# Optimization experiments

Hardware: AMD Instinct MI355X
Metric: run time of the kernel (lower is better)

The kernel has to match this reference:

```python
import jax, jax.numpy as jnp
import numpy as np

N_NODES = 100000
IN_CH = 128
HID = 128   # 2 * out_channels
OUT = 64
N_EDGES = 1600000


def gcn_conv(x, W, b, src, dst, n_nodes):
    """PyG GCNConv: add self-loops, symmetric normalization D^-1/2 (A+I) D^-1/2 X W + b."""
    h = x @ W  # [N, F_out]
    ones = jnp.ones(dst.shape[0], dtype=h.dtype)
    # degree of target nodes, +1 for self loop
    deg = jax.ops.segment_sum(ones, dst, num_segments=n_nodes) + 1.0
    dinv = jnp.where(deg > 0, jax.lax.rsqrt(deg), 0.0)  # [N]
    norm = dinv[src] * dinv[dst]  # [E]
    agg = jax.ops.segment_sum(h[src] * norm[:, None], dst, num_segments=n_nodes)
    # self-loop contribution: norm_ii = dinv_i^2 (avoids materializing extra edges)
    agg = agg + h * (dinv * dinv)[:, None]
    return agg + b


def setup_inputs() -> dict:
    key = jax.random.key(0)
    ks = jax.random.split(key, 8)
    x = jax.random.normal(ks[0], (N_NODES, IN_CH), dtype=jnp.float32)
    edge_index = jax.random.randint(ks[1], (2, N_EDGES), 0, N_NODES, dtype=jnp.int64)
    # Glorot-style params
    W1 = jax.random.normal(ks[2], (IN_CH, HID), dtype=jnp.float32) / np.sqrt(IN_CH)
    b1 = jnp.zeros((HID,), dtype=jnp.float32)
    W_mu = jax.random.normal(ks[3], (HID, OUT), dtype=jnp.float32) / np.sqrt(HID)
    b_mu = jnp.zeros((OUT,), dtype=jnp.float32)
    W_ls = jax.random.normal(ks[4], (HID, OUT), dtype=jnp.float32) / np.sqrt(HID)
    b_ls = jnp.zeros((OUT,), dtype=jnp.float32)
    return {"x": x, "edge_index": edge_index, "W1": W1, "b1": b1,
            "W_mu": W_mu, "b_mu": b_mu, "W_ls": W_ls, "b_ls": b_ls}


def reference(x, edge_index, W1, b1, W_mu, b_mu, W_ls, b_ls):
    src, dst = edge_index[0], edge_index[1]
    n = x.shape[0]
    h = jax.nn.relu(gcn_conv(x, W1, b1, src, dst, n))
    mu = gcn_conv(h, W_mu, b_mu, src, dst, n)
    logstd = gcn_conv(h, W_ls, b_ls, src, dst, n)
    return (mu, logstd)
```

## Files before the change

### kernel.cpp

```cpp
#include <hip/hip_runtime.h>
#include <hip/hip_bf16.h>
#include <stdint.h>

#define N_NODES 100000
#define IN_CH   128
#define HID     128
#define OUT_CH  64
#define N_EDGES 1600000

#define NB    196
#define NBLK  250
#define EPB   6400

typedef __attribute__((ext_vector_type(8))) short  bf16x8;
typedef __attribute__((ext_vector_type(4))) float  f32x4;


__device__ __forceinline__ unsigned short f2bf(float f) {
    unsigned int u = __float_as_uint(f);
    u = (u + 0x7fffu + ((u >> 16) & 1u)) >> 16;
    return (unsigned short)u;
}
__device__ __forceinline__ float bfl(unsigned int u) { return __uint_as_float(u << 16); }
__device__ __forceinline__ float bfh(unsigned int u) { return __uint_as_float(u & 0xffff0000u); }


__global__ __launch_bounds__(256) void k_phaseA(const int* __restrict__ dst,
                                                int* __restrict__ Cm) {
    __shared__ int hist[NB];
    int blk = blockIdx.x, t = threadIdx.x;
    if (t < NB) hist[t] = 0;
    __syncthreads();
    int base = blk * EPB;
#pragma unroll 5
    for (int k = 0; k < EPB / 256; k++) {
        int d = dst[base + k * 256 + t];
        atomicAdd(&hist[d >> 9], 1);
    }
    __syncthreads();
    if (t < NB) Cm[blk * NB + t] = hist[t];
}

__global__ __launch_bounds__(256) void k_scanBkt(int* __restrict__ Cm,
                                                 int* __restrict__ bktSum) {
    __shared__ int sdata[256];
    int b = blockIdx.x, t = threadIdx.x;
    int v = (t < NBLK) ? Cm[t * NB + b] : 0;
    sdata[t] = v;
    __syncthreads();
    int val = v;
    for (int off = 1; off < 256; off <<= 1) {
        int tmp = (t >= off) ? sdata[t - off] : 0;
        __syncthreads();
        val += tmp;
        sdata[t] = val;
        __syncthreads();
    }
    if (t < NBLK) Cm[t * NB + b] = val - v;
    if (t == 255) bktSum[b] = val;
}

__global__ __launch_bounds__(256) void k_scanBase(const int* __restrict__ bktSum,
                                                  int* __restrict__ bktBase) {
    __shared__ int sdata[256];
    int t = threadIdx.x;
    int v = (t < NB) ? bktSum[t] : 0;
    sdata[t] = v;
    __syncthreads();
    int val = v;
    for (int off = 1; off < 256; off <<= 1) {
        int tmp = (t >= off) ? sdata[t - off] : 0;
        __syncthreads();
        val += tmp;
        sdata[t] = val;
        __syncthreads();
    }
    if (t < NB) bktBase[t] = val - v;
    if (t == 0) bktBase[NB] = N_EDGES;
}

__global__ __launch_bounds__(256) void k_phaseB(const int* __restrict__ src,
                                                const int* __restrict__ dst,
                                                const int* __restrict__ Cm,
                                                const int* __restrict__ bktBase,
                                                unsigned int* __restrict__ bucketed) {
    __shared__ int offs[NB];
    int blk = blockIdx.x, t = threadIdx.x;
    if (t < NB) offs[t] = Cm[blk * NB + t] + bktBase[t];
    __syncthreads();
    int base = blk * EPB;
#pragma unroll 5
    for (int k = 0; k < EPB / 256; k++) {
        int e = base + k * 256 + t;
        int d = dst[e];
        int sv = src[e];
        int pos = atomicAdd(&offs[d >> 9], 1);
        bucketed[pos] = ((unsigned int)sv << 9) | (unsigned int)(d & 511);
    }
}

__global__ __launch_bounds__(512) void k_phaseC(const unsigned int* __restrict__ bucketed,
                                                const int* __restrict__ bktBase,
                                                int* __restrict__ rowptr,
                                                float* __restrict__ dinvg,
                                                int* __restrict__ csr_src) {
    __shared__ int cnt[512];
    __shared__ int cur[512];
    __shared__ int sdata[512];
    int b = blockIdx.x, t = threadIdx.x;
    int base = bktBase[b], endR = bktBase[b + 1];
    int nodeBase = b << 9;
    int nNodes = N_NODES - nodeBase;
    if (nNodes > 512) nNodes = 512;

    cnt[t] = 0;
    __syncthreads();
    for (int e = base + t; e < endR; e += 512)
        atomicAdd(&cnt[bucketed[e] & 511], 1);
    __syncthreads();

    int s = cnt[t];
    sdata[t] = s;
    __syncthreads();
    int val = s;
    for (int off = 1; off < 512; off <<= 1) {
        int tmp = (t >= off) ? sdata[t - off] : 0;
        __syncthreads();
        val += tmp;
        sdata[t] = val;
        __syncthreads();
    }
    cur[t] = val - s;
    if (t < nNodes) {
        rowptr[nodeBase + t] = base + val - s;
        dinvg[nodeBase + t] = rsqrtf((float)s + 1.0f);
    }
    if (b == NB - 1 && t == 0) rowptr[N_NODES] = N_EDGES;
    __syncthreads();

    for (int e = base + t; e < endR; e += 512) {
        unsigned int u = bucketed[e];
        int pos = base + atomicAdd(&cur[u & 511], 1);
        csr_src[pos] = (int)(u >> 9);
    }
}


__global__ __launch_bounds__(256) void k_prepW(const float* __restrict__ W1,
                                               const float* __restrict__ Wmu,
                                               const float* __restrict__ Wls,
                                               unsigned short* __restrict__ Wt1,
                                               unsigned short* __restrict__ WtC) {
    int idx = blockIdx.x * 256 + threadIdx.x;
    int n = idx >> 7, k = idx & 127;
    Wt1[idx] = f2bf(W1[k * 128 + n]);
    WtC[idx] = f2bf((n < 64) ? Wmu[k * 64 + n] : Wls[k * 64 + (n - 64)]);
}


#define LDA 136

__global__ __launch_bounds__(256) void k_gemm1(const float* __restrict__ X,
                                               const unsigned short* __restrict__ Wt,
                                               unsigned short* __restrict__ Y) {
    __shared__ unsigned short sA[128 * LDA];
    int t = threadIdx.x;
    int R0 = blockIdx.x * 128;
    int row = t >> 1, colb = (t & 1) * 64;
    bool valid = (R0 + row) < N_NODES;
    const float* Xr = X + (size_t)(R0 + row) * 128 + colb;
    unsigned short* dp = sA + row * LDA + colb;
#pragma unroll
    for (int j = 0; j < 16; j++) {
        float4 v = valid ? *(const float4*)(Xr + j * 4) : make_float4(0.f, 0.f, 0.f, 0.f);
        ushort4 o;
        o.x = f2bf(v.x); o.y = f2bf(v.y); o.z = f2bf(v.z); o.w = f2bf(v.w);
        *(ushort4*)(dp + j * 4) = o;
    }
    __syncthreads();

    int wv = t >> 6, l = t & 63;
    int quad = l >> 4, lm = l & 15;

    bf16x8 a[2][4];
#pragma unroll
    for (int mt = 0; mt < 2; mt++)
#pragma unroll
        for (int ks = 0; ks < 4; ks++)
            a[mt][ks] = *(const bf16x8*)(sA + (wv * 32 + mt * 16 + lm) * LDA +
                                         ks * 32 + quad * 8);

    f32x4 acc[2][8] = {};
#pragma unroll
    for (int nt = 0; nt < 8; nt++) {
        bf16x8 b[4];
        const unsigned short* Wp = Wt + (nt * 16 + lm) * 128 + quad * 8;
#pragma unroll
        for (int ks = 0; ks < 4; ks++)
            b[ks] = *(const bf16x8*)(Wp + ks * 32);
#pragma unroll
        for (int mt = 0; mt < 2; mt++) {
            f32x4 c = acc[mt][nt];
#pragma unroll
            for (int ks = 0; ks < 4; ks++)
                c = __builtin_amdgcn_mfma_f32_16x16x32_bf16(a[mt][ks], b[ks], c, 0, 0, 0);
            acc[mt][nt] = c;
        }
    }

    int rbase = R0 + wv * 32 + quad * 4;
#pragma unroll
    for (int mt = 0; mt < 2; mt++)
#pragma unroll
        for (int nt = 0; nt < 8; nt++)
#pragma unroll
            for (int reg = 0; reg < 4; reg++) {
                int r = rbase + mt * 16 + reg;
                if (r < N_NODES)
                    Y[(size_t)r * 128 + nt * 16 + lm] = f2bf(acc[mt][nt][reg]);
            }
}


__global__ __launch_bounds__(256) void k_agg1(const unsigned short* __restrict__ h0,
                                              const int* __restrict__ rowptr,
                                              const int* __restrict__ csr_src,
                                              const float* __restrict__ dinv,
                                              const float* __restrict__ b1,
                                              unsigned short* __restrict__ hb) {
    int lane = threadIdx.x & 63;
    int i = __builtin_amdgcn_readfirstlane(blockIdx.x * 4 + (threadIdx.x >> 6));
    int c2 = lane * 2;
    float di = dinv[i];
    unsigned int sv = *(const unsigned int*)(h0 + (size_t)i * 128 + c2);
    float ax = bfl(sv) * di * di, ay = bfh(sv) * di * di;
    int beg = rowptr[i], end = rowptr[i + 1];
    for (int p = beg; p < end; p += 16) {
        int s[16]; float n[16]; unsigned int r[16];
#pragma unroll
        for (int j = 0; j < 16; j++) {
            int q = p + j;
            s[j] = csr_src[q < end ? q : end - 1];
        }
#pragma unroll
        for (int j = 0; j < 16; j++) n[j] = dinv[s[j]];
#pragma unroll
        for (int j = 0; j < 16; j++)
            r[j] = *(const unsigned int*)(h0 + (size_t)s[j] * 128 + c2);
#pragma unroll
        for (int j = 0; j < 16; j++) n[j] = (p + j < end) ? n[j] * di : 0.f;
#pragma unroll
        for (int j = 0; j < 16; j++) {
            ax = fmaf(bfl(r[j]), n[j], ax);
            ay = fmaf(bfh(r[j]), n[j], ay);
        }
    }
    ax += b1[c2];
    ay += b1[c2 + 1];
    ax = ax > 0.f ? ax : 0.f;
    ay = ay > 0.f ? ay : 0.f;
    unsigned int pk = ((unsigned int)f2bf(ay) << 16) | (unsigned int)f2bf(ax);
    *(unsigned int*)(hb + (size_t)i * 128 + c2) = pk;
}


#define LDG 136

__global__ __launch_bounds__(256) void k_agg2g(const unsigned short* __restrict__ hb,
                                               const int* __restrict__ rowptr,
                                               const int* __restrict__ csr_src,
                                               const float* __restrict__ dinv,
                                               const unsigned short* __restrict__ WtC,
                                               const float* __restrict__ bmu,
                                               const float* __restrict__ bls,
                                               float* __restrict__ out) {
    __shared__ unsigned short g[16 * LDG];
    int t = threadIdx.x;
    int wv = t >> 6, lane = t & 63;
    int nodeBase = blockIdx.x * 16;
    int c2 = lane * 2;

#pragma unroll 1
    for (int j4 = 0; j4 < 4; j4++) {
        int i = __builtin_amdgcn_readfirstlane(nodeBase + wv * 4 + j4);
        float di = dinv[i];
        unsigned int sv = *(const unsigned int*)(hb + (size_t)i * 128 + c2);
        float ax = bfl(sv) * di * di, ay = bfh(sv) * di * di;
        int beg = rowptr[i], end = rowptr[i + 1];
        for (int p = beg; p < end; p += 16) {
            int s[16]; float n[16]; unsigned int r[16];
#pragma unroll
            for (int j = 0; j < 16; j++) {
                int q = p + j;
                s[j] = csr_src[q < end ? q : end - 1];
            }
#pragma unroll
            for (int j = 0; j < 16; j++) n[j] = dinv[s[j]];
#pragma unroll
            for (int j = 0; j < 16; j++)
                r[j] = *(const unsigned int*)(hb + (size_t)s[j] * 128 + c2);
#pragma unroll
            for (int j = 0; j < 16; j++) n[j] = (p + j < end) ? n[j] * di : 0.f;
#pragma unroll
            for (int j = 0; j < 16; j++) {
                ax = fmaf(bfl(r[j]), n[j], ax);
                ay = fmaf(bfh(r[j]), n[j], ay);
            }
        }
        unsigned int pk = ((unsigned int)f2bf(ay) << 16) | (unsigned int)f2bf(ax);
        *(unsigned int*)(g + (wv * 4 + j4) * LDG + c2) = pk;
    }
    __syncthreads();

    int quad = lane >> 4, lm = lane & 15;
    bf16x8 a[4];
#pragma unroll
    for (int ks = 0; ks < 4; ks++)
        a[ks] = *(const bf16x8*)(g + lm * LDG + ks * 32 + quad * 8);

#pragma unroll
    for (int nt2 = 0; nt2 < 2; nt2++) {
        int nt = wv * 2 + nt2;
        f32x4 acc = {};
        const unsigned short* Wp = WtC + (nt * 16 + lm) * 128 + quad * 8;
#pragma unroll
        for (int ks = 0; ks < 4; ks++) {
            bf16x8 b = *(const bf16x8*)(Wp + ks * 32);
            acc = __builtin_amdgcn_mfma_f32_16x16x32_bf16(a[ks], b, acc, 0, 0, 0);
        }
        int col = nt * 16 + lm;
#pragma unroll
        for (int reg = 0; reg < 4; reg++) {
            int row = nodeBase + quad * 4 + reg;
            float v = acc[reg];
            if (col < 64)
                out[(size_t)row * 64 + col] = v + bmu[col];
            else
                out[(size_t)N_NODES * 64 + (size_t)row * 64 + (col - 64)] = v + bls[col - 64];
        }
    }
}


extern "C" void kernel_launch(void* const* d_in, const int* in_sizes, int n_in,
                              void* d_out, int out_size, void* d_ws, size_t ws_size,
                              hipStream_t stream) {
    const float* x    = (const float*)d_in[0];
    const int*   ei   = (const int*)d_in[1];
    const float* W1   = (const float*)d_in[2];
    const float* b1   = (const float*)d_in[3];
    const float* Wmu  = (const float*)d_in[4];
    const float* bmu  = (const float*)d_in[5];
    const float* Wls  = (const float*)d_in[6];
    const float* bls  = (const float*)d_in[7];
    const int* src = ei;
    const int* dst = ei + N_EDGES;

    char* p = (char*)d_ws;
    unsigned short* bufA = (unsigned short*)p; p += (size_t)N_NODES * 128 * 2;
    unsigned short* bufH = (unsigned short*)p; p += (size_t)N_NODES * 128 * 2;
    unsigned short* Wt1  = (unsigned short*)p; p += 128 * 128 * 2;
    unsigned short* WtC  = (unsigned short*)p; p += 128 * 128 * 2;
    int*   Cm      = (int*)p;   p += (size_t)NBLK * NB * 4;
    int*   bktSum  = (int*)p;   p += 256 * 4;
    int*   bktBase = (int*)p;   p += 256 * 4;
    int*   rowptr  = (int*)p;   p += 400016;
    float* dinv    = (float*)p; p += 400000;
    unsigned int* bucketed = (unsigned int*)p; p += (size_t)N_EDGES * 4;
    int*   csr_src = (int*)p;   p += (size_t)N_EDGES * 4;

    k_phaseA<<<NBLK, 256, 0, stream>>>(dst, Cm);
    k_scanBkt<<<NB, 256, 0, stream>>>(Cm, bktSum);
    k_scanBase<<<1, 256, 0, stream>>>(bktSum, bktBase);
    k_phaseB<<<NBLK, 256, 0, stream>>>(src, dst, Cm, bktBase, bucketed);
    k_phaseC<<<NB, 512, 0, stream>>>(bucketed, bktBase, rowptr, dinv, csr_src);

    k_prepW<<<64, 256, 0, stream>>>(W1, Wmu, Wls, Wt1, WtC);

    int gblk = (N_NODES + 127) / 128;

    k_gemm1<<<gblk, 256, 0, stream>>>(x, Wt1, bufA);
    k_agg1<<<N_NODES / 4, 256, 0, stream>>>(bufA, rowptr, csr_src, dinv, b1, bufH);

    k_agg2g<<<N_NODES / 16, 256, 0, stream>>>(bufH, rowptr, csr_src, dinv,
                                              WtC, bmu, bls, (float*)d_out);
}
```

Measured before the change: 360.8 us.

## Slice feature matrices into 16-column planes for cache-local sparse aggregation

Result: slower. 756.1 us (+109.6%).

```diff
diff --git a/kernel.cpp b/kernel.cpp
--- a/kernel.cpp
+++ b/kernel.cpp
@@ -217,128 +217,159 @@
             for (int reg = 0; reg < 4; reg++) {
                 int r = rbase + mt * 16 + reg;
                 if (r < N_NODES)
-                    Y[(size_t)r * 128 + nt * 16 + lm] = f2bf(acc[mt][nt][reg]);
+                    Y[((size_t)nt * N_NODES + r) * 16 + lm] = f2bf(acc[mt][nt][reg]);
             }
 }
 
 
-__global__ __launch_bounds__(256) void k_agg1(const unsigned short* __restrict__ h0,
+template<int LAYER>
+__global__ __launch_bounds__(256) void k_aggs(const unsigned short* __restrict__ Hin,
                                               const int* __restrict__ rowptr,
                                               const int* __restrict__ csr_src,
                                               const float* __restrict__ dinv,
-                                              const float* __restrict__ b1,
-                                              unsigned short* __restrict__ hb) {
-    int lane = threadIdx.x & 63;
-    int i = __builtin_amdgcn_readfirstlane(blockIdx.x * 4 + (threadIdx.x >> 6));
-    int c2 = lane * 2;
-    float di = dinv[i];
-    unsigned int sv = *(const unsigned int*)(h0 + (size_t)i * 128 + c2);
-    float ax = bfl(sv) * di * di, ay = bfh(sv) * di * di;
-    int beg = rowptr[i], end = rowptr[i + 1];
-    for (int p = beg; p < end; p += 16) {
-        int s[16]; float n[16]; unsigned int r[16];
-#pragma unroll
-        for (int j = 0; j < 16; j++) {
-            int q = p + j;
-            s[j] = csr_src[q < end ? q : end - 1];
+                                              const float* __restrict__ bias,
+                                              unsigned short* __restrict__ Hout) {
+    int t = threadIdx.x;
+    int wv = t >> 6, l = t & 63;
+    int slice = blockIdx.x & 7;
+    int blkn = blockIdx.x >> 3;
+    int quad = l >> 2, ql = l & 3;
+    int i = blkn * 64 + wv * 16 + quad;
+    bool vnode = i < N_NODES;
+    int il = vnode ? i : 0;
+    const unsigned short* Hs = Hin + (size_t)slice * (N_NODES * 16);
+
+    float di = dinv[il];
+    int beg = vnode ? rowptr[il] : 0;
+    int end = vnode ? rowptr[il + 1] : 0;
+    int deg = end - beg;
+
+    int md = deg;
+    md = max(md, __shfl_xor(md, 4));
+    md = max(md, __shfl_xor(md, 8));
+    md = max(md, __shfl_xor(md, 16));
+    md = max(md, __shfl_xor(md, 32));
+    md = __builtin_amdgcn_readfirstlane(md);
+
+    uint2 sv = *(const uint2*)(Hs + (size_t)il * 16 + ql * 4);
+    float nn = di * di;
+    float a0 = bfl(sv.x) * nn, a1 = bfh(sv.x) * nn;
+    float a2 = bfl(sv.y) * nn, a3 = bfh(sv.y) * nn;
+
+    for (int p = 0; p < md; p += 8) {
+        int s[8]; float n[8]; uint2 r[8];
+#pragma unroll
+        for (int j = 0; j < 8; j++) {
+            int q = beg + p + j;
+            int qc = q < end ? q : end - 1;
+            qc = qc < 0 ? 0 : qc;
+            s[j] = __builtin_nontemporal_load(csr_src + qc);
         }
 #pragma unroll
-        for (int j = 0; j < 16; j++) n[j] = dinv[s[j]];
-#pragma unroll
-        for (int j = 0; j < 16; j++)
-            r[j] = *(const unsigned int*)(h0 + (size_t)s[j] * 128 + c2);
-#pragma unroll
-        for (int j = 0; j < 16; j++) n[j] = (p + j < end) ? n[j] * di : 0.f;
-#pragma unroll
-        for (int j = 0; j < 16; j++) {
-            ax = fmaf(bfl(r[j]), n[j], ax);
-            ay = fmaf(bfh(r[j]), n[j], ay);
+        for (int j = 0; j < 8; j++) n[j] = dinv[s[j]];
+#pragma unroll
+        for (int j = 0; j < 8; j++)
+            r[j] = *(const uint2*)(Hs + (size_t)s[j] * 16 + ql * 4);
+#pragma unroll
+        for (int j = 0; j < 8; j++) n[j] = (beg + p + j < end) ? n[j] * di : 0.f;
+#pragma unroll
+        for (int j = 0; j < 8; j++) {
+            a0 = fmaf(bfl(r[j].x), n[j], a0);
+            a1 = fmaf(bfh(r[j].x), n[j], a1);
+            a2 = fmaf(bfl(r[j].y), n[j], a2);
+            a3 = fmaf(bfh(r[j].y), n[j], a3);
         }
     }
-    ax += b1[c2];
-    ay += b1[c2 + 1];
-    ax = ax > 0.f ? ax : 0.f;
-    ay = ay > 0.f ? ay : 0.f;
-    unsigned int pk = ((unsigned int)f2bf(ay) << 16) | (unsigned int)f2bf(ax);
-    *(unsigned int*)(hb + (size_t)i * 128 + c2) = pk;
-}
-
-
-#define LDG 136
-
-__global__ __launch_bounds__(256) void k_agg2g(const unsigned short* __restrict__ hb,
-                                               const int* __restrict__ rowptr,
-                                               const int* __restrict__ csr_src,
-                                               const float* __restrict__ dinv,
-                                               const unsigned short* __restrict__ WtC,
+
+    if (!vnode) return;
+
+    if (LAYER == 1) {
+        const float4 bv = *(const float4*)(bias + slice * 16 + ql * 4);
+        a0 += bv.x; a1 += bv.y; a2 += bv.z; a3 += bv.w;
+        a0 = a0 > 0.f ? a0 : 0.f;
+        a1 = a1 > 0.f ? a1 : 0.f;
+        a2 = a2 > 0.f ? a2 : 0.f;
+        a3 = a3 > 0.f ? a3 : 0.f;
+        uint2 o;
+        o.x = ((unsigned int)f2bf(a1) << 16) | (unsigned int)f2bf(a0);
+        o.y = ((unsigned int)f2bf(a3) << 16) | (unsigned int)f2bf(a2);
+        *(uint2*)(Hout + ((size_t)slice * N_NODES + i) * 16 + ql * 4) = o;
+    } else {
+        uint2 o;
+        o.x = ((unsigned int)f2bf(a1) << 16) | (unsigned int)f2bf(a0);
+        o.y = ((unsigned int)f2bf(a3) << 16) | (unsigned int)f2bf(a2);
+        *(uint2*)(Hout + (size_t)i * 128 + slice * 16 + ql * 4) = o;
+    }
+}
+
+
+__global__ __launch_bounds__(256) void k_gemm2(const unsigned short* __restrict__ G,
+                                               const unsigned short* __restrict__ Wt,
                                                const float* __restrict__ bmu,
                                                const float* __restrict__ bls,
                                                float* __restrict__ out) {
-    __shared__ unsigned short g[16 * LDG];
+    __shared__ unsigned short sA[128 * LDA];
     int t = threadIdx.x;
-    int wv = t >> 6, lane = t & 63;
-    int nodeBase = blockIdx.x * 16;
-    int c2 = lane * 2;
-
-#pragma unroll 1
-    for (int j4 = 0; j4 < 4; j4++) {
-        int i = __builtin_amdgcn_readfirstlane(nodeBase + wv * 4 + j4);
-        float di = dinv[i];
-        unsigned int sv = *(const unsigned int*)(hb + (size_t)i * 128 + c2);
-        float ax = bfl(sv) * di * di, ay = bfh(sv) * di * di;
-        int beg = rowptr[i], end = rowptr[i + 1];
-        for (int p = beg; p < end; p += 16) {
-            int s[16]; float n[16]; unsigned int r[16];
-#pragma unroll
-            for (int j = 0; j < 16; j++) {
-                int q = p + j;
-                s[j] = csr_src[q < end ? q : end - 1];
-            }
-#pragma unroll
-            for (int j = 0; j < 16; j++) n[j] = dinv[s[j]];
-#pragma unroll
-            for (int j = 0; j < 16; j++)
-                r[j] = *(const unsigned int*)(hb + (size_t)s[j] * 128 + c2);
-#pragma unroll
-            for (int j = 0; j < 16; j++) n[j] = (p + j < end) ? n[j] * di : 0.f;
-#pragma unroll
-            for (int j = 0; j < 16; j++) {
-                ax = fmaf(bfl(r[j]), n[j], ax);
-                ay = fmaf(bfh(r[j]), n[j], ay);
+    int R0 = blockIdx.x * 128;
+    int row = t >> 1, colb = (t & 1) * 64;
+    bool valid = (R0 + row) < N_NODES;
+    const unsigned short* Gr = G + (size_t)(R0 + row) * 128 + colb;
+    unsigned short* dp = sA + row * LDA + colb;
+#pragma unroll
+    for (int j = 0; j < 8; j++) {
+        bf16x8 v = {0, 0, 0, 0, 0, 0, 0, 0};
+        if (valid) v = *(const bf16x8*)(Gr + j * 8);
+        *(bf16x8*)(dp + j * 8) = v;
+    }
+    __syncthreads();
+
+    int wv = t >> 6, l = t & 63;
+    int quad = l >> 4, lm = l & 15;
+
+    bf16x8 a[2][4];
+#pragma unroll
+    for (int mt = 0; mt < 2; mt++)
+#pragma unroll
+        for (int ks = 0; ks < 4; ks++)
+            a[mt][ks] = *(const bf16x8*)(sA + (wv * 32 + mt * 16 + lm) * LDA +
+                                         ks * 32 + quad * 8);
+
+    f32x4 acc[2][8] = {};
+#pragma unroll
+    for (int nt = 0; nt < 8; nt++) {
+        bf16x8 b[4];
+        const unsigned short* Wp = Wt + (nt * 16 + lm) * 128 + quad * 8;
+#pragma unroll
+        for (int ks = 0; ks < 4; ks++)
+            b[ks] = *(const bf16x8*)(Wp + ks * 32);
+#pragma unroll
+        for (int mt = 0; mt < 2; mt++) {
+            f32x4 c = acc[mt][nt];
+#pragma unroll
+            for (int ks = 0; ks < 4; ks++)
+                c = __builtin_amdgcn_mfma_f32_16x16x32_bf16(a[mt][ks], b[ks], c, 0, 0, 0);
+            acc[mt][nt] = c;
+        }
+    }
+
+    int rbase = R0 + wv * 32 + quad * 4;
+#pragma unroll
+    for (int mt = 0; mt < 2; mt++)
+#pragma unroll
+        for (int nt = 0; nt < 8; nt++) {
+            int col = nt * 16 + lm;
+#pragma unroll
+            for (int reg = 0; reg < 4; reg++) {
+                int r = rbase + mt * 16 + reg;
+                if (r < N_NODES) {
+                    float v = acc[mt][nt][reg];
+                    if (col < 64)
+                        out[(size_t)r * 64 + col] = v + bmu[col];
+                    else
+                        out[(size_t)N_NODES * 64 + (size_t)r * 64 + (col - 64)] = v + bls[col - 64];
+                }
             }
         }
-        unsigned int pk = ((unsigned int)f2bf(ay) << 16) | (unsigned int)f2bf(ax);
-        *(unsigned int*)(g + (wv * 4 + j4) * LDG + c2) = pk;
-    }
-    __syncthreads();
-
-    int quad = lane >> 4, lm = lane & 15;
-    bf16x8 a[4];
-#pragma unroll
-    for (int ks = 0; ks < 4; ks++)
-        a[ks] = *(const bf16x8*)(g + lm * LDG + ks * 32 + quad * 8);
-
-#pragma unroll
-    for (int nt2 = 0; nt2 < 2; nt2++) {
-        int nt = wv * 2 + nt2;
-        f32x4 acc = {};
-        const unsigned short* Wp = WtC + (nt * 16 + lm) * 128 + quad * 8;
-#pragma unroll
-        for (int ks = 0; ks < 4; ks++) {
-            bf16x8 b = *(const bf16x8*)(Wp + ks * 32);
-            acc = __builtin_amdgcn_mfma_f32_16x16x32_bf16(a[ks], b, acc, 0, 0, 0);
-        }
-        int col = nt * 16 + lm;
-#pragma unroll
-        for (int reg = 0; reg < 4; reg++) {
-            int row = nodeBase + quad * 4 + reg;
-            float v = acc[reg];
-            if (col < 64)
-                out[(size_t)row * 64 + col] = v + bmu[col];
-            else
-                out[(size_t)N_NODES * 64 + (size_t)row * 64 + (col - 64)] = v + bls[col - 64];
-        }
-    }
 }
 
 
@@ -378,10 +409,11 @@
     k_prepW<<<64, 256, 0, stream>>>(W1, Wmu, Wls, Wt1, WtC);
 
     int gblk = (N_NODES + 127) / 128;
+    int aggblk = ((N_NODES + 63) / 64) * 8;
 
     k_gemm1<<<gblk, 256, 0, stream>>>(x, Wt1, bufA);
-    k_agg1<<<N_NODES / 4, 256, 0, stream>>>(bufA, rowptr, csr_src, dinv, b1, bufH);
-
-    k_agg2g<<<N_NODES / 16, 256, 0, stream>>>(bufH, rowptr, csr_src, dinv,
-                                              WtC, bmu, bls, (float*)d_out);
-}
+    k_aggs<1><<<aggblk, 256, 0, stream>>>(bufA, rowptr, csr_src, dinv, b1, bufH);
+
+    k_aggs<2><<<aggblk, 256, 0, stream>>>(bufH, rowptr, csr_src, dinv, bmu, bufA);
+    k_gemm2<<<gblk, 256, 0, stream>>>(bufA, WtC, bmu, bls, (float*)d_out);
+}
```

## Fold source-side degree normalization into producers and drop per-edge dinv gathers

Applied to the files above, without the earlier changes.

New measurement: 348.2 us. 3.5% less time.

```diff
diff --git a/kernel.cpp b/kernel.cpp
--- a/kernel.cpp
+++ b/kernel.cpp
@@ -162,6 +162,7 @@
 
 __global__ __launch_bounds__(256) void k_gemm1(const float* __restrict__ X,
                                                const unsigned short* __restrict__ Wt,
+                                               const float* __restrict__ dinv,
                                                unsigned short* __restrict__ Y) {
     __shared__ unsigned short sA[128 * LDA];
     int t = threadIdx.x;
@@ -209,6 +210,14 @@
     }
 
     int rbase = R0 + wv * 32 + quad * 4;
+    float dv[2][4];
+#pragma unroll
+    for (int mt = 0; mt < 2; mt++)
+#pragma unroll
+        for (int reg = 0; reg < 4; reg++) {
+            int r = rbase + mt * 16 + reg;
+            dv[mt][reg] = (r < N_NODES) ? dinv[r] : 0.f;
+        }
 #pragma unroll
     for (int mt = 0; mt < 2; mt++)
 #pragma unroll
@@ -217,7 +226,7 @@
             for (int reg = 0; reg < 4; reg++) {
                 int r = rbase + mt * 16 + reg;
                 if (r < N_NODES)
-                    Y[(size_t)r * 128 + nt * 16 + lm] = f2bf(acc[mt][nt][reg]);
+                    Y[(size_t)r * 128 + nt * 16 + lm] = f2bf(acc[mt][nt][reg] * dv[mt][reg]);
             }
 }
 
@@ -233,32 +242,31 @@
     int c2 = lane * 2;
     float di = dinv[i];
     unsigned int sv = *(const unsigned int*)(h0 + (size_t)i * 128 + c2);
-    float ax = bfl(sv) * di * di, ay = bfh(sv) * di * di;
+    float ax = bfl(sv), ay = bfh(sv);
     int beg = rowptr[i], end = rowptr[i + 1];
-    for (int p = beg; p < end; p += 16) {
-        int s[16]; float n[16]; unsigned int r[16];
-#pragma unroll
-        for (int j = 0; j < 16; j++) {
+    for (int p = beg; p < end; p += 32) {
+        int s[32]; unsigned int r[32];
+#pragma unroll
+        for (int j = 0; j < 32; j++) {
             int q = p + j;
             s[j] = csr_src[q < end ? q : end - 1];
         }
 #pragma unroll
-        for (int j = 0; j < 16; j++) n[j] = dinv[s[j]];
-#pragma unroll
-        for (int j = 0; j < 16; j++)
+        for (int j = 0; j < 32; j++)
             r[j] = *(const unsigned int*)(h0 + (size_t)s[j] * 128 + c2);
 #pragma unroll
-        for (int j = 0; j < 16; j++) n[j] = (p + j < end) ? n[j] * di : 0.f;
-#pragma unroll
-        for (int j = 0; j < 16; j++) {
-            ax = fmaf(bfl(r[j]), n[j], ax);
-            ay = fmaf(bfh(r[j]), n[j], ay);
-        }
-    }
-    ax += b1[c2];
-    ay += b1[c2 + 1];
+        for (int j = 0; j < 32; j++) {
+            unsigned int v = (p + j < end) ? r[j] : 0u;
+            ax += bfl(v);
+            ay += bfh(v);
+        }
+    }
+    ax = ax * di + b1[c2];
+    ay = ay * di + b1[c2 + 1];
     ax = ax > 0.f ? ax : 0.f;
     ay = ay > 0.f ? ay : 0.f;
+    ax *= di;
+    ay *= di;
     unsigned int pk = ((unsigned int)f2bf(ay) << 16) | (unsigned int)f2bf(ax);
     *(unsigned int*)(hb + (size_t)i * 128 + c2) = pk;
 }
@@ -285,28 +293,27 @@
         int i = __builtin_amdgcn_readfirstlane(nodeBase + wv * 4 + j4);
         float di = dinv[i];
         unsigned int sv = *(const unsigned int*)(hb + (size_t)i * 128 + c2);
-        float ax = bfl(sv) * di * di, ay = bfh(sv) * di * di;
+        float ax = bfl(sv), ay = bfh(sv);
         int beg = rowptr[i], end = rowptr[i + 1];
-        for (int p = beg; p < end; p += 16) {
-            int s[16]; float n[16]; unsigned int r[16];
-#pragma unroll
-            for (int j = 0; j < 16; j++) {
+        for (int p = beg; p < end; p += 32) {
+            int s[32]; unsigned int r[32];
+#pragma unroll
+            for (int j = 0; j < 32; j++) {
                 int q = p + j;
                 s[j] = csr_src[q < end ? q : end - 1];
             }
 #pragma unroll
-            for (int j = 0; j < 16; j++) n[j] = dinv[s[j]];
-#pragma unroll
-            for (int j = 0; j < 16; j++)
+            for (int j = 0; j < 32; j++)
                 r[j] = *(const unsigned int*)(hb + (size_t)s[j] * 128 + c2);
 #pragma unroll
-            for (int j = 0; j < 16; j++) n[j] = (p + j < end) ? n[j] * di : 0.f;
-#pragma unroll
-            for (int j = 0; j < 16; j++) {
-                ax = fmaf(bfl(r[j]), n[j], ax);
-                ay = fmaf(bfh(r[j]), n[j], ay);
+            for (int j = 0; j < 32; j++) {
+                unsigned int v = (p + j < end) ? r[j] : 0u;
+                ax += bfl(v);
+                ay += bfh(v);
             }
         }
+        ax *= di;
+        ay *= di;
         unsigned int pk = ((unsigned int)f2bf(ay) << 16) | (unsigned int)f2bf(ax);
         *(unsigned int*)(g + (wv * 4 + j4) * LDG + c2) = pk;
     }
@@ -379,7 +386,7 @@
 
     int gblk = (N_NODES + 127) / 128;
 
-    k_gemm1<<<gblk, 256, 0, stream>>>(x, Wt1, bufA);
+    k_gemm1<<<gblk, 256, 0, stream>>>(x, Wt1, dinv, bufA);
     k_agg1<<<N_NODES / 4, 256, 0, stream>>>(bufA, rowptr, csr_src, dinv, b1, bufH);
 
     k_agg2g<<<N_NODES / 16, 256, 0, stream>>>(bufH, rowptr, csr_src, dinv,
```
